# Kernel optimization log

Measured on AMD Instinct MI355X. Metric: run time of the kernel, lower is better.

Reference implementation:

```python
import jax, jax.numpy as jnp
import numpy as np

N_NODES = 50000
N_EDGES = 600000
N_LABEL = 200000
IN_CH = 128
OUT_CH = 128
K_HOPS = 2


def setup_inputs() -> dict:
    key = jax.random.key(0)
    ks = jax.random.split(key, 9)
    x = jax.random.normal(ks[0], (N_NODES, IN_CH), dtype=jnp.float32)
    edge_index = jax.random.randint(ks[1], (2, N_EDGES), 0, N_NODES)
    edge_label_index = jax.random.randint(ks[2], (2, N_LABEL), 0, N_NODES)
    conv_weight = jax.random.normal(ks[3], (OUT_CH, IN_CH), dtype=jnp.float32) * 0.05
    conv_bias = jax.random.normal(ks[4], (OUT_CH,), dtype=jnp.float32) * 0.05
    w1 = jax.random.normal(ks[5], (OUT_CH // 2, OUT_CH), dtype=jnp.float32) * 0.05
    b1 = jax.random.normal(ks[6], (OUT_CH // 2,), dtype=jnp.float32) * 0.05
    w2 = jax.random.normal(ks[7], (1, OUT_CH // 2), dtype=jnp.float32) * 0.05
    b2 = jax.random.normal(ks[8], (1,), dtype=jnp.float32) * 0.05
    return {"x": x, "edge_index": edge_index, "edge_label_index": edge_label_index,
            "conv_weight": conv_weight, "conv_bias": conv_bias,
            "w1": w1, "b1": b1, "w2": w2, "b2": b2}


def reference(x, edge_index, edge_label_index, conv_weight, conv_bias, w1, b1, w2, b2):
    n = x.shape[0]
    # gcn_norm with self-loops: A_hat = D^{-1/2} (A + I) D^{-1/2}
    loop = jnp.arange(n, dtype=edge_index.dtype)
    src = jnp.concatenate([edge_index[0], loop])  # message sources
    dst = jnp.concatenate([edge_index[1], loop])  # aggregation targets
    deg = jax.ops.segment_sum(jnp.ones_like(dst, dtype=x.dtype), dst, num_segments=n)
    dinv = jnp.where(deg > 0, jax.lax.rsqrt(deg), 0.0)
    w = dinv[src] * dinv[dst]  # [E+N] edge weights

    # K-hop propagation: h <- A_hat h, repeated K times (SGConv)
    h = x
    for _ in range(K_HOPS):
        h = jax.ops.segment_sum(h[src] * w[:, None], dst, num_segments=n)
    z = h @ conv_weight.T + conv_bias  # [N, out_channels]

    # decode: gather endpoint embeddings, multiply, tiny MLP (dropout inactive at eval)
    s = z[edge_label_index[0]] * z[edge_label_index[1]]  # [E_label, out]
    h1 = jax.nn.relu(s @ w1.T + b1)
    r = (h1 @ w2.T + b2).sum(axis=-1)  # [E_label]
    return r
```

## Files before the change

### kernel.cpp

```cpp
#include <hip/hip_runtime.h>

#define N_CH 128

typedef _Float16 half8  __attribute__((ext_vector_type(8)));
typedef _Float16 half4v __attribute__((ext_vector_type(4)));
typedef float    floatx4 __attribute__((ext_vector_type(4)));


__global__ void k_prep(int* __restrict__ cnt,
                       const float* __restrict__ W,  _Float16* __restrict__ wh,
                       const float* __restrict__ W1, _Float16* __restrict__ w1h,
                       int n) {
    int i = blockIdx.x * blockDim.x + threadIdx.x;
    if (i < n) cnt[i] = 0;
    int nw4  = N_CH * N_CH / 4;
    int nw14 = 64 * N_CH / 4;
    if (i < nw4) {
        float4 v = ((const float4*)W)[i];
        half4v o;
        o[0] = (_Float16)v.x; o[1] = (_Float16)v.y; o[2] = (_Float16)v.z; o[3] = (_Float16)v.w;
        ((half4v*)wh)[i] = o;
    } else if (i < nw4 + nw14) {
        int j = i - nw4;
        float4 v = ((const float4*)W1)[j];
        half4v o;
        o[0] = (_Float16)v.x; o[1] = (_Float16)v.y; o[2] = (_Float16)v.z; o[3] = (_Float16)v.w;
        ((half4v*)w1h)[j] = o;
    }
}


__global__ void k_count(const int* __restrict__ dst, int* __restrict__ cnt, int E) {
    int e = blockIdx.x * blockDim.x + threadIdx.x;
    if (e < E) atomicAdd(&cnt[dst[e]], 1);
}

__global__ __launch_bounds__(1024) void k_scan1(const int* __restrict__ cnt,
                                                int* __restrict__ offs,
                                                int* __restrict__ bsum, int n) {
    __shared__ int ssum[16];
    int tid = threadIdx.x;
    int lane = tid & 63, wid = tid >> 6;
    int i = blockIdx.x * 1024 + tid;
    int v = (i < n) ? ((cnt[i] + 7) & ~7) : 0;
    int x = v;
    #pragma unroll
    for (int off = 1; off < 64; off <<= 1) {
        int y = __shfl_up(x, off, 64);
        if (lane >= off) x += y;
    }
    if (lane == 63) ssum[wid] = x;
    __syncthreads();
    if (wid == 0 && lane < 16) {
        int s = ssum[lane];
        #pragma unroll
        for (int off = 1; off < 16; off <<= 1) {
            int y = __shfl_up(s, off, 64);
            if (lane >= off) s += y;
        }
        ssum[lane] = s;
    }
    __syncthreads();
    int waveoff = (wid > 0) ? ssum[wid - 1] : 0;
    int incl = x + waveoff;
    if (i < n) offs[i] = incl - v;
    if (tid == 1023) bsum[blockIdx.x] = incl;
}

__global__ __launch_bounds__(256) void k_scan3(const int* __restrict__ cnt,
                                               int* __restrict__ offs,
                                               const int* __restrict__ bsum,
                                               int* __restrict__ cur,
                                               float* __restrict__ dinv,
                                               unsigned short* __restrict__ csr,
                                               int n, int nb) {
    __shared__ int sbb[64];
    int tid = threadIdx.x;
    if (tid < 64) {
        int v = (tid < nb) ? bsum[tid] : 0;
        int x = v;
        #pragma unroll
        for (int off = 1; off < 64; off <<= 1) {
            int y = __shfl_up(x, off, 64);
            if (tid >= off) x += y;
        }
        sbb[tid] = x - v;
    }
    __syncthreads();
    int i = blockIdx.x * blockDim.x + tid;
    if (i < n) {
        int o = offs[i] + sbb[i >> 10];
        offs[i] = o;
        cur[i]  = o;
        int c = cnt[i];
        dinv[i] = rsqrtf((float)(c + 1));
        int cp = (c + 7) & ~7;
        unsigned short zn = (unsigned short)n;
        for (int j = c; j < cp; ++j) csr[o + j] = zn;
    }
}

__global__ void k_fill(const int* __restrict__ src, const int* __restrict__ dst,
                       int* __restrict__ cur, unsigned short* __restrict__ csr, int E) {
    int e = blockIdx.x * blockDim.x + threadIdx.x;
    if (e < E) {
        int p = atomicAdd(&cur[dst[e]], 1);
        csr[p] = (unsigned short)src[e];
    }
}


__global__ void k_scale(const float* __restrict__ x, const float* __restrict__ dinv,
                        _Float16* __restrict__ u0, _Float16* __restrict__ u1, int n) {
    int i = blockIdx.x * blockDim.x + threadIdx.x;
    int nx4 = n * (N_CH / 4);
    if (i < nx4) {
        float d = dinv[i >> 5];
        float4 v = ((const float4*)x)[i];
        half4v o;
        o[0] = (_Float16)(d * v.x); o[1] = (_Float16)(d * v.y);
        o[2] = (_Float16)(d * v.z); o[3] = (_Float16)(d * v.w);
        ((half4v*)u0)[i] = o;
    } else if (i < nx4 + 64) {
        int j = i - nx4;
        half4v zz; zz[0] = (_Float16)0.f; zz[1] = (_Float16)0.f; zz[2] = (_Float16)0.f; zz[3] = (_Float16)0.f;
        _Float16* dst16 = (j < 32) ? u0 : u1;
        ((half4v*)(dst16 + (size_t)n * N_CH))[j & 31] = zz;
    }
}


__global__ __launch_bounds__(256) void k_hop8(const _Float16* __restrict__ hin,
                                              _Float16* __restrict__ hout,
                                              const int* __restrict__ offs,
                                              const int* __restrict__ cnt,
                                              const float* __restrict__ dinv,
                                              const unsigned short* __restrict__ csr,
                                              int n, int squared, int nblk) {
    int pass = (blockIdx.x >= nblk) ? 1 : 0;
    int bid  = blockIdx.x - pass * nblk;
    int tid  = threadIdx.x;
    int node = bid * 32 + (tid >> 3);
    int c8   = tid & 7;
    if (node >= n) return;
    int cbase = pass * 8 + c8;
    float di = dinv[node];
    float sc = squared ? di * di : di;
    int s0 = offs[node];
    int cp = (cnt[node] + 7) & ~7;
    const uint4* qlst = (const uint4*)(csr + s0);
    half8 self = ((const half8*)(hin + (size_t)node * N_CH))[cbase];
    float acc[8];
    #pragma unroll
    for (int j = 0; j < 8; ++j) acc[j] = (float)self[j];
    int nq = cp >> 3;
    for (int q = 0; q < nq; ++q) {
        uint4 pk = qlst[q];
        int idx[8];
        idx[0] = pk.x & 0xFFFF; idx[1] = pk.x >> 16;
        idx[2] = pk.y & 0xFFFF; idx[3] = pk.y >> 16;
        idx[4] = pk.z & 0xFFFF; idx[5] = pk.z >> 16;
        idx[6] = pk.w & 0xFFFF; idx[7] = pk.w >> 16;
        half8 u[8];
        #pragma unroll
        for (int i = 0; i < 8; ++i)
            u[i] = ((const half8*)(hin + (size_t)idx[i] * N_CH))[cbase];
        #pragma unroll
        for (int i = 0; i < 8; ++i)
            #pragma unroll
            for (int j = 0; j < 8; ++j) acc[j] += (float)u[i][j];
    }
    half8 o;
    #pragma unroll
    for (int j = 0; j < 8; ++j) o[j] = (_Float16)(sc * acc[j]);
    ((half8*)(hout + (size_t)node * N_CH))[cbase] = o;
}


__global__ __launch_bounds__(256) void k_zlin_mfma(const _Float16* __restrict__ h,
                                                   const _Float16* __restrict__ wh,
                                                   const float* __restrict__ bc,
                                                   _Float16* __restrict__ z, int n) {
    __shared__ half8 wls[128 * 16];
    int tid = threadIdx.x;
    int lane = tid & 63, w = tid >> 6;
    int quad = lane >> 4, m16 = lane & 15;
    int nb = blockIdx.x * 64;
    #pragma unroll
    for (int i = 0; i < 8; ++i) {
        int g = tid + 256 * i;
        int r = g >> 4, c = g & 15;
        wls[r * 16 + (c ^ (r & 15))] = ((const half8*)wh)[g];
    }
    int arow = nb + w * 16 + m16;
    const half8* hrow = (const half8*)(h + (size_t)arow * N_CH);
    half8 a[4];
    #pragma unroll
    for (int kk = 0; kk < 4; ++kk) a[kk] = hrow[kk * 4 + quad];
    __syncthreads();
    int outnode0 = nb + w * 16 + quad * 4;
    #pragma unroll
    for (int jt = 0; jt < 8; ++jt) {
        floatx4 acc = {0.f, 0.f, 0.f, 0.f};
        #pragma unroll
        for (int kk = 0; kk < 4; ++kk) {
            int r = jt * 16 + m16;
            half8 bfr = wls[r * 16 + ((kk * 4 + quad) ^ m16)];
            acc = __builtin_amdgcn_mfma_f32_16x16x32_f16(a[kk], bfr, acc, 0, 0, 0);
        }
        int j = jt * 16 + m16;
        float bias = bc[j];
        #pragma unroll
        for (int reg = 0; reg < 4; ++reg) {
            int node = outnode0 + reg;
            if (node < n) z[(size_t)node * N_CH + j] = (_Float16)(acc[reg] + bias);
        }
    }
}


__global__ __launch_bounds__(256) void k_decode_mfma(const _Float16* __restrict__ z,
        const int* __restrict__ ai, const int* __restrict__ bi,
        const _Float16* __restrict__ w1h, const float* __restrict__ b1,
        const float* __restrict__ w2, const float* __restrict__ b2,
        float* __restrict__ out, int m) {
    __shared__ half8 w1ls[64 * 16];
    __shared__ half8 sls[64 * 16];
    int tid = threadIdx.x;
    int lane = tid & 63, w = tid >> 6;
    int quad = lane >> 4, m16 = lane & 15;
    int pbase = blockIdx.x * 64;
    #pragma unroll
    for (int i = 0; i < 4; ++i) {
        int g = tid + 256 * i;
        int r = g >> 4, c = g & 15;
        w1ls[r * 16 + (c ^ (r & 15))] = ((const half8*)w1h)[g];
    }
    int pidx = pbase + w * 16 + m16;
    if (pidx >= m) pidx = m - 1;
    int idxa = ai[pidx];
    int idxb = bi[pidx];
    int ia[4], ib[4];
    #pragma unroll
    for (int it = 0; it < 4; ++it) {
        int p = it * 4 + quad;
        ia[it] = __shfl(idxa, p, 64);
        ib[it] = __shfl(idxb, p, 64);
    }
    half8 za[4], zb[4];
    #pragma unroll
    for (int it = 0; it < 4; ++it) {
        za[it] = ((const half8*)(z + (size_t)ia[it] * N_CH))[m16];
        zb[it] = ((const half8*)(z + (size_t)ib[it] * N_CH))[m16];
    }
    #pragma unroll
    for (int it = 0; it < 4; ++it) {
        half8 s8 = za[it] * zb[it];
        int pp = w * 16 + it * 4 + quad;
        sls[pp * 16 + (m16 ^ (pp & 15))] = s8;
    }
    __syncthreads();
    half8 a[4];
    #pragma unroll
    for (int kk = 0; kk < 4; ++kk)
        a[kk] = sls[(w * 16 + m16) * 16 + ((kk * 4 + quad) ^ m16)];
    float rsum[4] = {0.f, 0.f, 0.f, 0.f};
    #pragma unroll
    for (int jt = 0; jt < 4; ++jt) {
        floatx4 acc = {0.f, 0.f, 0.f, 0.f};
        #pragma unroll
        for (int kk = 0; kk < 4; ++kk) {
            int r = jt * 16 + m16;
            half8 bfr = w1ls[r * 16 + ((kk * 4 + quad) ^ m16)];
            acc = __builtin_amdgcn_mfma_f32_16x16x32_f16(a[kk], bfr, acc, 0, 0, 0);
        }
        int j = jt * 16 + m16;
        float b1j = b1[j], w2j = w2[j];
        #pragma unroll
        for (int reg = 0; reg < 4; ++reg) {
            float v = fmaxf(acc[reg] + b1j, 0.f) * w2j;
            v += __shfl_xor(v, 1, 64);
            v += __shfl_xor(v, 2, 64);
            v += __shfl_xor(v, 4, 64);
            v += __shfl_xor(v, 8, 64);
            rsum[reg] += v;
        }
    }
    if (m16 == 0) {
        float bb = b2[0];
        #pragma unroll
        for (int reg = 0; reg < 4; ++reg) {
            int gp = pbase + w * 16 + quad * 4 + reg;
            if (gp < m) out[gp] = rsum[reg] + bb;
        }
    }
}


extern "C" void kernel_launch(void* const* d_in, const int* in_sizes, int n_in,
                              void* d_out, int out_size, void* d_ws, size_t ws_size,
                              hipStream_t stream) {
    const float* x   = (const float*)d_in[0];
    const int*   ei  = (const int*)d_in[1];
    const int*   eli = (const int*)d_in[2];
    const float* W   = (const float*)d_in[3];
    const float* bc  = (const float*)d_in[4];
    const float* W1  = (const float*)d_in[5];
    const float* b1  = (const float*)d_in[6];
    const float* w2  = (const float*)d_in[7];
    const float* b2  = (const float*)d_in[8];
    float* out = (float*)d_out;

    const int N = in_sizes[0] / N_CH;
    const int E = in_sizes[1] / 2;
    const int M = in_sizes[2] / 2;

    const int* src = ei;
    const int* dst = ei + E;
    const int* ai  = eli;
    const int* bi  = eli + M;

    _Float16* hb0 = (_Float16*)d_ws;
    _Float16* hb1 = hb0 + (size_t)(N + 1) * N_CH;
    _Float16* wh  = hb1 + (size_t)(N + 1) * N_CH;
    _Float16* w1h = wh + 16384;
    unsigned short* csr = (unsigned short*)(w1h + 8192);
    int*   cnt  = (int*)(csr + (size_t)E + 8 * (size_t)N);
    int*   off  = cnt + N;
    int*   cur  = off + N;
    float* dnv  = (float*)(cur + N);
    int*   bsum = (int*)(dnv + N);

    int nb = (N + 1023) / 1024;
    k_prep<<<(N + 255) / 256, 256, 0, stream>>>(cnt, W, wh, W1, w1h, N);
    k_count<<<(E + 255) / 256, 256, 0, stream>>>(dst, cnt, E);
    k_scan1<<<nb, 1024, 0, stream>>>(cnt, off, bsum, N);
    k_scan3<<<(N + 255) / 256, 256, 0, stream>>>(cnt, off, bsum, cur, dnv, csr, N, nb);
    k_fill<<<(E + 255) / 256, 256, 0, stream>>>(src, dst, cur, csr, E);
    int sc_work = N * (N_CH / 4) + 64;
    k_scale<<<(sc_work + 255) / 256, 256, 0, stream>>>(x, dnv, hb0, hb1, N);

    int nblk = (N + 31) / 32;
    k_hop8<<<2 * nblk, 256, 0, stream>>>(hb0, hb1, off, cnt, dnv, csr, N, 1, nblk);
    k_hop8<<<2 * nblk, 256, 0, stream>>>(hb1, hb0, off, cnt, dnv, csr, N, 0, nblk);

    k_zlin_mfma<<<(N + 63) / 64, 256, 0, stream>>>(hb0, wh, bc, hb1, N);

    k_decode_mfma<<<(M + 63) / 64, 256, 0, stream>>>(hb1, ai, bi, w1h, b1, w2, b2, out, M);
}
```

Measured before the change: 225.3 us.

## Store features in channel-planar slabs, fuse CSR fill with scaling, use nontemporal hints

Node features are now stored in four planes of 32 channels, each with (N+1)*4 half8 entries. Each of the four hop passes gathers from one contiguous 3.2MB slab, which is more likely to stay resident in cache during random neighbour gathers. The CSR fill and the x scaling kernels are merged into one launch. Nontemporal loads and stores are added for the CSR stream and the outputs. The z-linear kernel is updated to read the new planar layout. In exchange, every hop now reads the CSR index list four times instead of twice.

```diff
diff --git a/kernel.cpp b/kernel.cpp
--- a/kernel.cpp
+++ b/kernel.cpp
@@ -5,6 +5,7 @@
 typedef _Float16 half8  __attribute__((ext_vector_type(8)));
 typedef _Float16 half4v __attribute__((ext_vector_type(4)));
 typedef float    floatx4 __attribute__((ext_vector_type(4)));
+typedef unsigned int uint4v __attribute__((ext_vector_type(4)));
 
 
 __global__ void k_prep(int* __restrict__ cnt,
@@ -100,71 +101,85 @@
     }
 }
 
-__global__ void k_fill(const int* __restrict__ src, const int* __restrict__ dst,
-                       int* __restrict__ cur, unsigned short* __restrict__ csr, int E) {
-    int e = blockIdx.x * blockDim.x + threadIdx.x;
-    if (e < E) {
-        int p = atomicAdd(&cur[dst[e]], 1);
-        csr[p] = (unsigned short)src[e];
-    }
-}
-
-
-__global__ void k_scale(const float* __restrict__ x, const float* __restrict__ dinv,
-                        _Float16* __restrict__ u0, _Float16* __restrict__ u1, int n) {
-    int i = blockIdx.x * blockDim.x + threadIdx.x;
-    int nx4 = n * (N_CH / 4);
-    if (i < nx4) {
-        float d = dinv[i >> 5];
-        float4 v = ((const float4*)x)[i];
-        half4v o;
-        o[0] = (_Float16)(d * v.x); o[1] = (_Float16)(d * v.y);
-        o[2] = (_Float16)(d * v.z); o[3] = (_Float16)(d * v.w);
-        ((half4v*)u0)[i] = o;
-    } else if (i < nx4 + 64) {
-        int j = i - nx4;
-        half4v zz; zz[0] = (_Float16)0.f; zz[1] = (_Float16)0.f; zz[2] = (_Float16)0.f; zz[3] = (_Float16)0.f;
-        _Float16* dst16 = (j < 32) ? u0 : u1;
-        ((half4v*)(dst16 + (size_t)n * N_CH))[j & 31] = zz;
-    }
-}
-
-
-__global__ __launch_bounds__(256) void k_hop8(const _Float16* __restrict__ hin,
+
+__global__ __launch_bounds__(256) void k_fillscale(
+        const int* __restrict__ src, const int* __restrict__ dst,
+        int* __restrict__ cur, unsigned short* __restrict__ csr, int E,
+        const float* __restrict__ x, const float* __restrict__ dinv,
+        _Float16* __restrict__ u0, _Float16* __restrict__ u1, int n, int FB) {
+    int b = blockIdx.x;
+    int tid = threadIdx.x;
+    if (b < FB) {
+        int e = b * 256 + tid;
+        if (e < E) {
+            int p = atomicAdd(&cur[dst[e]], 1);
+            csr[p] = (unsigned short)src[e];
+        }
+        return;
+    }
+    int i = (b - FB) * 256 + tid;
+    size_t ps = (size_t)(n + 1) * 4;
+    int tot = n * 16;
+    if (i < tot) {
+        int node = i >> 4, chunk = i & 15;
+        float d = dinv[node];
+        float4 v0 = ((const float4*)x)[node * 32 + chunk * 2];
+        float4 v1 = ((const float4*)x)[node * 32 + chunk * 2 + 1];
+        half8 o;
+        o[0] = (_Float16)(d * v0.x); o[1] = (_Float16)(d * v0.y);
+        o[2] = (_Float16)(d * v0.z); o[3] = (_Float16)(d * v0.w);
+        o[4] = (_Float16)(d * v1.x); o[5] = (_Float16)(d * v1.y);
+        o[6] = (_Float16)(d * v1.z); o[7] = (_Float16)(d * v1.w);
+        __builtin_nontemporal_store(o,
+            &((half8*)u0)[(size_t)(chunk >> 2) * ps + (size_t)node * 4 + (chunk & 3)]);
+    } else if (i < tot + 32) {
+        int j = i - tot;
+        _Float16* d16 = (j < 16) ? u0 : u1;
+        int c = j & 15;
+        half8 zz;
+        #pragma unroll
+        for (int q = 0; q < 8; ++q) zz[q] = (_Float16)0.f;
+        ((half8*)d16)[(size_t)(c >> 2) * ps + (size_t)n * 4 + (c & 3)] = zz;
+    }
+}
+
+
+__global__ __launch_bounds__(256) void k_hop4(const _Float16* __restrict__ hin,
                                               _Float16* __restrict__ hout,
                                               const int* __restrict__ offs,
                                               const int* __restrict__ cnt,
                                               const float* __restrict__ dinv,
                                               const unsigned short* __restrict__ csr,
                                               int n, int squared, int nblk) {
-    int pass = (blockIdx.x >= nblk) ? 1 : 0;
+    int pass = blockIdx.x / nblk;
     int bid  = blockIdx.x - pass * nblk;
     int tid  = threadIdx.x;
-    int node = bid * 32 + (tid >> 3);
-    int c8   = tid & 7;
+    int node = bid * 64 + (tid >> 2);
     if (node >= n) return;
-    int cbase = pass * 8 + c8;
+    int c = tid & 3;
+    size_t ps = (size_t)(n + 1) * 4;
+    const half8* hp = (const half8*)hin + (size_t)pass * ps + c;
     float di = dinv[node];
     float sc = squared ? di * di : di;
     int s0 = offs[node];
     int cp = (cnt[node] + 7) & ~7;
-    const uint4* qlst = (const uint4*)(csr + s0);
-    half8 self = ((const half8*)(hin + (size_t)node * N_CH))[cbase];
+    const uint4v* qlst = (const uint4v*)(csr + s0);
+    half8 self = hp[(size_t)node * 4];
     float acc[8];
     #pragma unroll
     for (int j = 0; j < 8; ++j) acc[j] = (float)self[j];
     int nq = cp >> 3;
     for (int q = 0; q < nq; ++q) {
-        uint4 pk = qlst[q];
+        uint4v pk = __builtin_nontemporal_load(&qlst[q]);
         int idx[8];
-        idx[0] = pk.x & 0xFFFF; idx[1] = pk.x >> 16;
-        idx[2] = pk.y & 0xFFFF; idx[3] = pk.y >> 16;
-        idx[4] = pk.z & 0xFFFF; idx[5] = pk.z >> 16;
-        idx[6] = pk.w & 0xFFFF; idx[7] = pk.w >> 16;
+        idx[0] = pk[0] & 0xFFFF; idx[1] = pk[0] >> 16;
+        idx[2] = pk[1] & 0xFFFF; idx[3] = pk[1] >> 16;
+        idx[4] = pk[2] & 0xFFFF; idx[5] = pk[2] >> 16;
+        idx[6] = pk[3] & 0xFFFF; idx[7] = pk[3] >> 16;
         half8 u[8];
         #pragma unroll
         for (int i = 0; i < 8; ++i)
-            u[i] = ((const half8*)(hin + (size_t)idx[i] * N_CH))[cbase];
+            u[i] = hp[(size_t)idx[i] * 4];
         #pragma unroll
         for (int i = 0; i < 8; ++i)
             #pragma unroll
@@ -173,7 +188,8 @@
     half8 o;
     #pragma unroll
     for (int j = 0; j < 8; ++j) o[j] = (_Float16)(sc * acc[j]);
-    ((half8*)(hout + (size_t)node * N_CH))[cbase] = o;
+    half8* op = (half8*)hout + (size_t)pass * ps + c;
+    __builtin_nontemporal_store(o, &op[(size_t)node * 4]);
 }
 
 
@@ -193,10 +209,12 @@
         wls[r * 16 + (c ^ (r & 15))] = ((const half8*)wh)[g];
     }
     int arow = nb + w * 16 + m16;
-    const half8* hrow = (const half8*)(h + (size_t)arow * N_CH);
+    size_t ps = (size_t)(n + 1) * 4;
+    const half8* hb8 = (const half8*)h;
     half8 a[4];
     #pragma unroll
-    for (int kk = 0; kk < 4; ++kk) a[kk] = hrow[kk * 4 + quad];
+    for (int kk = 0; kk < 4; ++kk)
+        a[kk] = hb8[(size_t)kk * ps + (size_t)arow * 4 + quad];
     __syncthreads();
     int outnode0 = nb + w * 16 + quad * 4;
     #pragma unroll
@@ -336,13 +354,16 @@
     k_count<<<(E + 255) / 256, 256, 0, stream>>>(dst, cnt, E);
     k_scan1<<<nb, 1024, 0, stream>>>(cnt, off, bsum, N);
     k_scan3<<<(N + 255) / 256, 256, 0, stream>>>(cnt, off, bsum, cur, dnv, csr, N, nb);
-    k_fill<<<(E + 255) / 256, 256, 0, stream>>>(src, dst, cur, csr, E);
-    int sc_work = N * (N_CH / 4) + 64;
-    k_scale<<<(sc_work + 255) / 256, 256, 0, stream>>>(x, dnv, hb0, hb1, N);
-
-    int nblk = (N + 31) / 32;
-    k_hop8<<<2 * nblk, 256, 0, stream>>>(hb0, hb1, off, cnt, dnv, csr, N, 1, nblk);
-    k_hop8<<<2 * nblk, 256, 0, stream>>>(hb1, hb0, off, cnt, dnv, csr, N, 0, nblk);
+
+    int FB = (E + 255) / 256;
+    int sw = N * 16 + 32;
+    int SB = (sw + 255) / 256;
+    k_fillscale<<<FB + SB, 256, 0, stream>>>(src, dst, cur, csr, E,
+                                             x, dnv, hb0, hb1, N, FB);
+
+    int nblk4 = (N + 63) / 64;
+    k_hop4<<<4 * nblk4, 256, 0, stream>>>(hb0, hb1, off, cnt, dnv, csr, N, 1, nblk4);
+    k_hop4<<<4 * nblk4, 256, 0, stream>>>(hb1, hb0, off, cnt, dnv, csr, N, 0, nblk4);
 
     k_zlin_mfma<<<(N + 63) / 64, 256, 0, stream>>>(hb0, wh, bc, hb1, N);
 
```

After: 238.0 us. 1.06x slower.
